# Performance work log

Measured on AMD Instinct MI355X. Metric: run time of the kernel, lower is better.

The kernel has to match this reference:

```python
import jax, jax.numpy as jnp
import numpy as np
from jax import lax

KH = KW = 3
STRIDE = (1, 1)
PAD = (1, 1)

def setup_inputs() -> dict:
    key = jax.random.key(0)
    k1, k2, k3 = jax.random.split(key, 3)
    B_, C, H, W = 16, 128, 56, 56
    O, R = 256, 16
    Kflat = C * KH * KW
    x = jax.random.normal(k1, (B_, C, H, W), dtype=jnp.float32)
    # kaiming_normal_ fan_out for A: std = sqrt(2/out_channels)
    A = jax.random.normal(k2, (O, R), dtype=jnp.float32) * np.float32(np.sqrt(2.0 / O))
    # kaiming_normal_ fan_in for B: std = sqrt(2/kernel_flat_dim)
    Bm = jax.random.normal(k3, (R, Kflat), dtype=jnp.float32) * np.float32(np.sqrt(2.0 / Kflat))
    return {"x": x, "A": A, "B": Bm}

def reference(x, A, B):
    b, c, h, w = x.shape
    h_out = (h + 2 * PAD[0] - KH) // STRIDE[0] + 1
    w_out = (w + 2 * PAD[1] - KW) // STRIDE[1] + 1
    # im2col: [B, C*KH*KW, H_out, W_out]; feature order (c, kh, kw) matches torch Unfold
    patches = lax.conv_general_dilated_patches(
        x, filter_shape=(KH, KW), window_strides=STRIDE,
        padding=((PAD[0], PAD[0]), (PAD[1], PAD[1])))
    patches = patches.reshape(b, c * KH * KW, h_out * w_out)  # [B, K, L]
    tmp = jnp.einsum('rk,bkl->brl', B, patches)               # rank-limited matmul
    out = jnp.einsum('or,brl->bol', A, tmp)                   # [B, O, L]
    return out.reshape(b, A.shape[0], h_out, w_out)
```

## Files before the change

kernel.cpp:

```cpp
#include <hip/hip_runtime.h>
#include <hip/hip_bf16.h>


#define Bn 16
#define Cc 128
#define Hh 56
#define Ww 56
#define Ll (Hh * Ww)
#define Rr 16
#define Oo 256
#define KF (Cc * 9)
#define HB 2

__device__ __forceinline__ float bf16_bits(unsigned short u) {
    return __uint_as_float(((unsigned)u) << 16);
}

template<bool BF>
__device__ __forceinline__ float ld(const void* __restrict__ p, size_t i) {
    if constexpr (BF) return bf16_bits(((const unsigned short*)p)[i]);
    else              return ((const float*)p)[i];
}

__device__ __forceinline__ bool detect_bf16(const void* __restrict__ p) {
    const unsigned* w = (const unsigned*)p;
    int c = 0;
#pragma unroll
    for (int i = 0; i < 32; ++i) {
        const unsigned e = (w[i] >> 7) & 0xFFu;
        c += (e >= 96u && e <= 144u) ? 1 : 0;
    }
    return c >= 20;
}

__global__ __launch_bounds__(256) void prep_kernel(
    const void* __restrict__ A, const void* __restrict__ Bm,
    float* __restrict__ Bt, float* __restrict__ Afp)
{
    const bool ab = detect_bf16(A);
    const bool bb = detect_bf16(Bm);
    const int i = blockIdx.x * 256 + threadIdx.x;
    if (i < KF * Rr) {
        const int k = i >> 4, r = i & 15;
        Bt[i] = bb ? bf16_bits(((const unsigned short*)Bm)[r * KF + k])
                   : ((const float*)Bm)[r * KF + k];
    }
    if (i < Oo * Rr) {
        Afp[i] = ab ? bf16_bits(((const unsigned short*)A)[i])
                    : ((const float*)A)[i];
    }
}

template<bool XB>
__device__ __forceinline__ void main_body(
    const void* __restrict__ x,
    const float* __restrict__ Bt,
    const float* __restrict__ Afp,
    float* __restrict__ out,
    float (* __restrict__ part)[4][Rr][64],
    float (* __restrict__ tmp2)[64][17])
{
    const int tid  = threadIdx.x;
    const int lane = tid & 63;
    const int wv   = __builtin_amdgcn_readfirstlane(tid >> 6);
    const int cs   = wv & 3;
    const int rh   = wv >> 2;
    const int h0   = blockIdx.x * HB;
    const int b    = blockIdx.y;
    const int w    = lane;
    const bool wok = (w < Ww);
    const int  wcl = wok ? w : (Ww - 1);

    float a[HB][3][8];
#pragma unroll
    for (int row = 0; row < HB; ++row)
#pragma unroll
        for (int dw = 0; dw < 3; ++dw)
#pragma unroll
            for (int j = 0; j < 8; ++j) a[row][dw][j] = 0.f;

    const size_t xbase = (size_t)b * Cc * Ll + (size_t)(cs * 32) * Ll;
    const float* btb   = Bt + (size_t)(cs * 32 * 9) * Rr + rh * 8;

    size_t rowb[HB + 2];
    bool   hv[HB + 2];
#pragma unroll
    for (int rr = 0; rr < HB + 2; ++rr) {
        const int hh  = h0 - 1 + rr;
        hv[rr] = (hh >= 0) & (hh < Hh);
        const int hcl = hv[rr] ? hh : (hh < 0 ? 0 : Hh - 1);
        rowb[rr] = xbase + (size_t)(hcl * Ww) + (size_t)wcl;
    }

    for (int cc = 0; cc < 32; ++cc) {
        const size_t coff = (size_t)cc * Ll;
        float xv[HB + 2];
#pragma unroll
        for (int rr = 0; rr < HB + 2; ++rr) {
            const float v = ld<XB>(x, rowb[rr] + coff);
            xv[rr] = hv[rr] ? v : 0.f;
        }
        const float* bt = btb + (size_t)(cc * 9) * Rr;
#pragma unroll
        for (int dh = 0; dh < 3; ++dh) {
            const float x0 = xv[dh];
            const float x1 = xv[dh + 1];
#pragma unroll
            for (int dw = 0; dw < 3; ++dw) {
                const float* bp = bt + (size_t)(dh * 3 + dw) * Rr;
#pragma unroll
                for (int j = 0; j < 8; ++j) {
                    const float bv = bp[j];
                    a[0][dw][j] += bv * x0;
                    a[1][dw][j] += bv * x1;
                }
            }
        }
    }

#pragma unroll
    for (int row = 0; row < HB; ++row)
#pragma unroll
    for (int j = 0; j < 8; ++j) {
        const float up = __shfl(a[row][0][j], w - 1);
        const float dn = __shfl(a[row][2][j], w + 1);
        float s = a[row][1][j];
        s += (w > 0)      ? up : 0.f;
        s += (w < Ww - 1) ? dn : 0.f;
        part[row][cs][rh * 8 + j][lane] = s;
    }
    __syncthreads();

    {
        const int px = tid & 63;
        const int rr = (tid >> 6) & 7;
#pragma unroll
        for (int row = 0; row < HB; ++row)
#pragma unroll
        for (int t = 0; t < 2; ++t) {
            const int r = rr + t * 8;
            tmp2[row][px][r] = part[row][0][r][px] + part[row][1][r][px]
                             + part[row][2][r][px] + part[row][3][r][px];
        }
    }
    __syncthreads();

    float tv[HB][Rr];
#pragma unroll
    for (int row = 0; row < HB; ++row)
#pragma unroll
        for (int r = 0; r < Rr; ++r) tv[row][r] = tmp2[row][lane][r];

    const size_t obase = (size_t)b * Oo * Ll + (size_t)(h0 * Ww) + (size_t)w;
#pragma unroll 4
    for (int j = 0; j < 32; ++j) {
        const int o = wv * 32 + j;
        const float* Ao = Afp + (size_t)o * Rr;
        float s0 = 0.f, s1 = 0.f;
#pragma unroll
        for (int r = 0; r < Rr; ++r) {
            const float av = Ao[r];
            s0 += av * tv[0][r];
            s1 += av * tv[1][r];
        }
        if (wok) {
            out[obase + (size_t)o * Ll]      = s0;
            out[obase + (size_t)o * Ll + Ww] = s1;
        }
    }
}

__global__ __launch_bounds__(512, 4) void fused_big(
    const void* __restrict__ x,
    const float* __restrict__ Bt,
    const float* __restrict__ Afp,
    float* __restrict__ out)
{
    __shared__ float part[HB][4][Rr][64];
    __shared__ float tmp2[HB][64][17];
    if (detect_bf16(x)) main_body<true >(x, Bt, Afp, out, part, tmp2);
    else                main_body<false>(x, Bt, Afp, out, part, tmp2);
}

__global__ __launch_bounds__(256) void fused_fallback(
    const void* __restrict__ x, const void* __restrict__ A,
    const void* __restrict__ Bm, float* __restrict__ out)
{
    const bool xb = detect_bf16(x);
    const bool ab = detect_bf16(A);
    const bool bb = detect_bf16(Bm);
    const int gid = blockIdx.x * 256 + threadIdx.x;
    const int b = gid / Ll;
    const int l = gid - b * Ll;
    const int h = l / Ww, w = l - h * Ww;
    float acc[Rr];
#pragma unroll
    for (int r = 0; r < Rr; ++r) acc[r] = 0.f;
    const size_t xbase = (size_t)b * Cc * Ll;
    for (int c = 0; c < Cc; ++c) {
        const size_t xc = xbase + (size_t)c * Ll;
        float xv[9];
#pragma unroll
        for (int dh = 0; dh < 3; ++dh) {
            const int hh = h + dh - 1;
            const bool hok = (hh >= 0) & (hh < Hh);
#pragma unroll
            for (int dw = 0; dw < 3; ++dw) {
                const int ww = w + dw - 1;
                const bool ok = hok & (ww >= 0) & (ww < Ww);
                const size_t idx = xc + (size_t)(hh * Ww + ww);
                xv[dh*3+dw] = ok ? (xb ? bf16_bits(((const unsigned short*)x)[idx])
                                       : ((const float*)x)[idx]) : 0.f;
            }
        }
#pragma unroll
        for (int r = 0; r < Rr; ++r) {
            const size_t bo = (size_t)r * KF + (size_t)c * 9;
            float s = acc[r];
#pragma unroll
            for (int i = 0; i < 9; ++i)
                s += (bb ? bf16_bits(((const unsigned short*)Bm)[bo+i])
                         : ((const float*)Bm)[bo+i]) * xv[i];
            acc[r] = s;
        }
    }
    const size_t obase = (size_t)b * Oo * Ll + (size_t)l;
    for (int o = 0; o < Oo; ++o) {
        float s = 0.f;
#pragma unroll
        for (int r = 0; r < Rr; ++r)
            s += (ab ? bf16_bits(((const unsigned short*)A)[o*Rr+r])
                     : ((const float*)A)[o*Rr+r]) * acc[r];
        out[obase + (size_t)o * Ll] = s;
    }
}

extern "C" void kernel_launch(void* const* d_in, const int* in_sizes, int n_in,
                              void* d_out, int out_size, void* d_ws, size_t ws_size,
                              hipStream_t stream) {
    const void* x  = d_in[0];
    const void* A  = d_in[1];
    const void* Bm = d_in[2];
    for (int i = 0; i < n_in && i < 3; ++i) {
        const int s = in_sizes[i];
        if      (s == Bn * Cc * Ll) x  = d_in[i];
        else if (s == Oo * Rr)      A  = d_in[i];
        else if (s == Rr * KF)      Bm = d_in[i];
    }
    float* out = (float*)d_out;

    const size_t need = (size_t)(KF * Rr + Oo * Rr) * sizeof(float);
    if (ws_size >= need) {
        float* Bt  = (float*)d_ws;
        float* Afp = Bt + KF * Rr;
        prep_kernel<<<dim3((KF * Rr + 255) / 256), 256, 0, stream>>>(A, Bm, Bt, Afp);
        fused_big<<<dim3(Hh / HB, Bn), 512, 0, stream>>>(x, Bt, Afp, out);
    } else {
        fused_fallback<<<dim3((Bn * Ll) / 256), 256, 0, stream>>>(x, A, Bm, out);
    }
}
```

Before: 120.6 us.

## Stage B weights in LDS, double-buffer x loads, use 32-bit indexing

Each block now copies the whole transposed B matrix (72 KB) into shared memory and reads it with float4 LDS loads instead of scalar global loads. The channel loop is unrolled by two with register double-buffering, so x values for channel cc+2 are prefetched while channel cc is computed. Index arithmetic moves from size_t to 32-bit unsigned, and the later reduction buffers reuse the same shared memory. The 72 KB LDS allocation per block limits how many blocks fit per CU, which may reduce occupancy compared with the launch_bounds target of 4.

```diff
diff --git a/kernel.cpp b/kernel.cpp
--- a/kernel.cpp
+++ b/kernel.cpp
@@ -17,7 +17,7 @@
 }
 
 template<bool BF>
-__device__ __forceinline__ float ld(const void* __restrict__ p, size_t i) {
+__device__ __forceinline__ float ld(const void* __restrict__ p, unsigned i) {
     if constexpr (BF) return bf16_bits(((const unsigned short*)p)[i]);
     else              return ((const float*)p)[i];
 }
@@ -51,14 +51,45 @@
     }
 }
 
+#define CONV_BODY(CC, XBUF)                                                  \
+    {                                                                        \
+        float xv[HB + 2];                                                    \
+        _Pragma("unroll")                                                    \
+        for (int rr = 0; rr < HB + 2; ++rr) xv[rr] = XBUF[rr];               \
+        const int ccn = ((CC) + 2 < 32) ? (CC) + 2 : (CC);                   \
+        const unsigned coffn = (unsigned)(ccn * Ll);                         \
+        _Pragma("unroll")                                                    \
+        for (int rr = 0; rr < HB + 2; ++rr) {                                \
+            const float v = ld<XB>(x, rowb[rr] + coffn);                     \
+            XBUF[rr] = hv[rr] ? v : 0.f;                                     \
+        }                                                                    \
+        const float* bw = Bw + (CC) * 144;                                   \
+        _Pragma("unroll")                                                    \
+        for (int dh = 0; dh < 3; ++dh) {                                     \
+            const float x0 = xv[dh], x1 = xv[dh + 1];                        \
+            _Pragma("unroll")                                                \
+            for (int dw = 0; dw < 3; ++dw) {                                 \
+                const float4 b0 = *(const float4*)(bw + (dh*3+dw)*16);       \
+                const float4 b1 = *(const float4*)(bw + (dh*3+dw)*16 + 4);   \
+                a[0][dw][0] += b0.x * x0;  a[1][dw][0] += b0.x * x1;         \
+                a[0][dw][1] += b0.y * x0;  a[1][dw][1] += b0.y * x1;         \
+                a[0][dw][2] += b0.z * x0;  a[1][dw][2] += b0.z * x1;         \
+                a[0][dw][3] += b0.w * x0;  a[1][dw][3] += b0.w * x1;         \
+                a[0][dw][4] += b1.x * x0;  a[1][dw][4] += b1.x * x1;         \
+                a[0][dw][5] += b1.y * x0;  a[1][dw][5] += b1.y * x1;         \
+                a[0][dw][6] += b1.z * x0;  a[1][dw][6] += b1.z * x1;         \
+                a[0][dw][7] += b1.w * x0;  a[1][dw][7] += b1.w * x1;         \
+            }                                                                \
+        }                                                                    \
+    }
+
 template<bool XB>
 __device__ __forceinline__ void main_body(
     const void* __restrict__ x,
     const float* __restrict__ Bt,
     const float* __restrict__ Afp,
     float* __restrict__ out,
-    float (* __restrict__ part)[4][Rr][64],
-    float (* __restrict__ tmp2)[64][17])
+    float* smem)
 {
     const int tid  = threadIdx.x;
     const int lane = tid & 63;
@@ -71,6 +102,15 @@
     const bool wok = (w < Ww);
     const int  wcl = wok ? w : (Ww - 1);
 
+    {
+        float4* dst = (float4*)smem;
+        const float4* src = (const float4*)Bt;
+#pragma unroll
+        for (int i = 0; i < 9; ++i) dst[tid + i * 512] = src[tid + i * 512];
+    }
+    __syncthreads();
+    const float* Bw = smem + (cs * 32) * 144 + rh * 8;
+
     float a[HB][3][8];
 #pragma unroll
     for (int row = 0; row < HB; ++row)
@@ -79,44 +119,34 @@
 #pragma unroll
             for (int j = 0; j < 8; ++j) a[row][dw][j] = 0.f;
 
-    const size_t xbase = (size_t)b * Cc * Ll + (size_t)(cs * 32) * Ll;
-    const float* btb   = Bt + (size_t)(cs * 32 * 9) * Rr + rh * 8;
-
-    size_t rowb[HB + 2];
-    bool   hv[HB + 2];
+    const unsigned xbase = (unsigned)(b * Cc * Ll + (cs * 32) * Ll);
+
+    unsigned rowb[HB + 2];
+    bool     hv[HB + 2];
 #pragma unroll
     for (int rr = 0; rr < HB + 2; ++rr) {
         const int hh  = h0 - 1 + rr;
         hv[rr] = (hh >= 0) & (hh < Hh);
         const int hcl = hv[rr] ? hh : (hh < 0 ? 0 : Hh - 1);
-        rowb[rr] = xbase + (size_t)(hcl * Ww) + (size_t)wcl;
-    }
-
-    for (int cc = 0; cc < 32; ++cc) {
-        const size_t coff = (size_t)cc * Ll;
-        float xv[HB + 2];
-#pragma unroll
-        for (int rr = 0; rr < HB + 2; ++rr) {
-            const float v = ld<XB>(x, rowb[rr] + coff);
-            xv[rr] = hv[rr] ? v : 0.f;
-        }
-        const float* bt = btb + (size_t)(cc * 9) * Rr;
-#pragma unroll
-        for (int dh = 0; dh < 3; ++dh) {
-            const float x0 = xv[dh];
-            const float x1 = xv[dh + 1];
-#pragma unroll
-            for (int dw = 0; dw < 3; ++dw) {
-                const float* bp = bt + (size_t)(dh * 3 + dw) * Rr;
-#pragma unroll
-                for (int j = 0; j < 8; ++j) {
-                    const float bv = bp[j];
-                    a[0][dw][j] += bv * x0;
-                    a[1][dw][j] += bv * x1;
-                }
-            }
-        }
-    }
+        rowb[rr] = xbase + (unsigned)(hcl * Ww) + (unsigned)wcl;
+    }
+
+    float xbA[HB + 2], xbB[HB + 2];
+#pragma unroll
+    for (int rr = 0; rr < HB + 2; ++rr) {
+        const float v0 = ld<XB>(x, rowb[rr]);
+        xbA[rr] = hv[rr] ? v0 : 0.f;
+        const float v1 = ld<XB>(x, rowb[rr] + (unsigned)Ll);
+        xbB[rr] = hv[rr] ? v1 : 0.f;
+    }
+    for (int t = 0; t < 16; ++t) {
+        CONV_BODY(2 * t,     xbA)
+        CONV_BODY(2 * t + 1, xbB)
+    }
+
+    __syncthreads();
+    float (*part)[4][Rr][64] = (float(*)[4][Rr][64])smem;
+    float (*tmp2)[64][17]    = (float(*)[64][17])(smem + HB*4*Rr*64);
 
 #pragma unroll
     for (int row = 0; row < HB; ++row)
@@ -176,10 +206,9 @@
     const float* __restrict__ Afp,
     float* __restrict__ out)
 {
-    __shared__ float part[HB][4][Rr][64];
-    __shared__ float tmp2[HB][64][17];
-    if (detect_bf16(x)) main_body<true >(x, Bt, Afp, out, part, tmp2);
-    else                main_body<false>(x, Bt, Afp, out, part, tmp2);
+    __shared__ __align__(16) float smem[KF * Rr];
+    if (detect_bf16(x)) main_body<true >(x, Bt, Afp, out, smem);
+    else                main_body<false>(x, Bt, Afp, out, smem);
 }
 
 __global__ __launch_bounds__(256) void fused_fallback(
```

After: 148.9 us. 23.5% more time.
